# Optimization experiments

Measured on AMD Instinct MI355X. Metric: run time of the kernel, lower is better.

Reference implementation:

```python
import jax, jax.numpy as jnp
import numpy as np

EMB = 1024
HEADS = 16
QKV = 64
INNER = 2816  # 256 * ceil(2*1024*4/3 / 256)


def rms_norm(x, w, eps=1e-6):
    xf = x.astype(jnp.float32)
    n = xf * jax.lax.rsqrt(jnp.mean(xf * xf, axis=-1, keepdims=True) + eps)
    return n.astype(x.dtype) * w


def setup_inputs() -> dict:
    key = jax.random.key(0)
    ks = jax.random.split(key, 12)
    s = 0.02
    return {
        "x": jax.random.normal(ks[0], (4, 2048, EMB), dtype=jnp.float32),
        "Wq": jax.random.normal(ks[1], (HEADS * QKV, EMB), dtype=jnp.float32) * s,
        "Wk": jax.random.normal(ks[2], (HEADS * QKV, EMB), dtype=jnp.float32) * s,
        "Wv": jax.random.normal(ks[3], (HEADS * QKV, EMB), dtype=jnp.float32) * s,
        "Wc": jax.random.normal(ks[4], (EMB, HEADS * QKV), dtype=jnp.float32) * s,
        "bc": jnp.zeros((EMB,), dtype=jnp.float32),
        "g1": jnp.ones((EMB,), dtype=jnp.float32),
        "g2": jnp.ones((EMB,), dtype=jnp.float32),
        "L1": jax.random.normal(ks[5], (INNER, EMB), dtype=jnp.float32) * s,
        "L2": jax.random.normal(ks[6], (INNER, EMB), dtype=jnp.float32) * s,
        "L3": jax.random.normal(ks[7], (EMB, INNER), dtype=jnp.float32) * s,
    }


def reference(x, Wq, Wk, Wv, Wc, bc, g1, g2, L1, L2, L3):
    B, N, D = x.shape
    # QKV projections (torch Linear: y = x @ W.T), split into heads: [B,H,N,dk]
    q = (x @ Wq.T).reshape(B, N, HEADS, QKV).transpose(0, 2, 1, 3)
    k = (x @ Wk.T).reshape(B, N, HEADS, QKV).transpose(0, 2, 1, 3)
    v = (x @ Wv.T).reshape(B, N, HEADS, QKV).transpose(0, 2, 1, 3)
    # attention: explicit score matrix [B,H,N,N]
    score = jnp.einsum("bhnd,bhmd->bhnm", q, k) / jnp.sqrt(jnp.float32(QKV))
    weights = jax.nn.softmax(score, axis=-1)
    out = jnp.einsum("bhnm,bhmd->bhnd", weights, v)
    out = out.transpose(0, 2, 1, 3).reshape(B, N, HEADS * QKV)
    mha = out @ Wc.T + bc
    h = rms_norm(x + mha, g1)
    # parallel gated MLP: silu(h@L1.T) * (h@L2.T) @ L3.T
    ff = (jax.nn.silu(h @ L1.T) * (h @ L2.T)) @ L3.T
    return rms_norm(h + ff, g2)
```

## Files before the change

kernel.cpp:

```cpp
#include <hip/hip_runtime.h>
#include <hip/hip_bf16.h>


#define EMB   1024
#define HEADS 16
#define DK    64
#define INNER 2816
#define BATCH 4
#define NTOK  2048
#define MROWS (BATCH * NTOK)

#define QSCALE 0.18033688011112042f

typedef short bf16x8 __attribute__((ext_vector_type(8)));
typedef short s16x4  __attribute__((ext_vector_type(4)));
typedef float f32x4  __attribute__((ext_vector_type(4)));

typedef const void __attribute__((address_space(1)))* gas_cvp;
typedef void       __attribute__((address_space(3)))* las_vp;

__device__ __forceinline__ short to_bf16(float f) {
  union { float f; unsigned u; } x; x.f = f;
  unsigned r = x.u + 0x7FFFu + ((x.u >> 16) & 1u);
  return (short)(r >> 16);
}

__device__ __forceinline__ unsigned cvt_pk_bf16(float a, float b) {
  unsigned r;
  asm("v_cvt_pk_bf16_f32 %0, %1, %2" : "=v"(r) : "v"(a), "v"(b));
  return r;
}

__device__ __forceinline__ void gld16(void* lds, const void* g) {
  __builtin_amdgcn_global_load_lds((gas_cvp)g, (las_vp)lds, 16, 0, 0);
}

__global__ __launch_bounds__(256, 4)
void cvtk(const float* __restrict__ s, short* __restrict__ d, int n4) {
  int i = blockIdx.x * 256 + threadIdx.x;
  if (i < n4) {
    float4 v = ((const float4*)s)[i];
    s16x4 o;
    o[0] = to_bf16(v.x); o[1] = to_bf16(v.y);
    o[2] = to_bf16(v.z); o[3] = to_bf16(v.w);
    ((s16x4*)d)[i] = o;
  }
}

__global__ __launch_bounds__(256, 4)
void cvt_inter(const float* __restrict__ L1, const float* __restrict__ L2,
               short* __restrict__ d) {
  int i = blockIdx.x * 256 + threadIdx.x;
  if (i >= INNER * 256) return;
  int row = i >> 8, c4 = i & 255;
  float4 v1 = ((const float4*)L1)[i];
  float4 v2 = ((const float4*)L2)[i];
  s16x4 o1, o2;
  o1[0]=to_bf16(v1.x); o1[1]=to_bf16(v1.y); o1[2]=to_bf16(v1.z); o1[3]=to_bf16(v1.w);
  o2[0]=to_bf16(v2.x); o2[1]=to_bf16(v2.y); o2[2]=to_bf16(v2.z); o2[3]=to_bf16(v2.w);
  ((s16x4*)d)[(size_t)(2 * row) * 256 + c4]     = o1;
  ((s16x4*)d)[(size_t)(2 * row + 1) * 256 + c4] = o2;
}

template<int MODE>
__global__ __launch_bounds__(256, 2)
void gemm_bt(const short* __restrict__ A, const short* __restrict__ Bw,
             int M, int N, int K,
             void* __restrict__ out0, void* __restrict__ out1,
             void* __restrict__ out2,
             const float* __restrict__ aux0, const float* __restrict__ aux1)
{
  __shared__ short At[128 * 64];
  __shared__ short Bt[128 * 64];
  const int t = threadIdx.x;
  const int lane = t & 63;
  const int l15 = lane & 15, lhi = lane >> 4;
  const int w  = t >> 6;
  const int wm = (w >> 1) << 6;
  const int wn = (w & 1) << 6;
  const int tilesN = N >> 7;
  const int m0 = (blockIdx.x / tilesN) << 7;
  const int n0 = (blockIdx.x % tilesN) << 7;

  const int r = t >> 3;
  const int p = t & 7;
  const int psrc = p ^ (r & 7);
  const short* Ag = A  + (size_t)(m0 + r) * K + psrc * 8;
  const short* Bg = Bw + (size_t)(n0 + r) * K + psrc * 8;

  f32x4 acc[4][4];
  const f32x4 fz = {0.f, 0.f, 0.f, 0.f};
#pragma unroll
  for (int i = 0; i < 4; i++)
#pragma unroll
    for (int j = 0; j < 4; j++) acc[i][j] = fz;

  int aoff[2][4], boff[2][4];
#pragma unroll
  for (int kk = 0; kk < 2; kk++)
#pragma unroll
    for (int mt = 0; mt < 4; mt++) {
      int ra = wm + mt * 16 + l15;
      aoff[kk][mt] = ra * 128 + ((kk * 64 + lhi * 16) ^ ((ra & 7) << 4));
      int rb = wn + mt * 16 + l15;
      boff[kk][mt] = rb * 128 + ((kk * 64 + lhi * 16) ^ ((rb & 7) << 4));
    }

  for (int k0 = 0; k0 < K; k0 += 64) {
#pragma unroll
    for (int i = 0; i < 4; i++) {
      gld16((char*)At + t * 16 + i * 4096, Ag + (size_t)i * 32 * K + k0);
      gld16((char*)Bt + t * 16 + i * 4096, Bg + (size_t)i * 32 * K + k0);
    }
    __syncthreads();
#pragma unroll
    for (int kk = 0; kk < 2; kk++) {
      bf16x8 a[4], b[4];
#pragma unroll
      for (int mt = 0; mt < 4; mt++)
        a[mt] = *(const bf16x8*)((const char*)At + aoff[kk][mt]);
#pragma unroll
      for (int nt = 0; nt < 4; nt++)
        b[nt] = *(const bf16x8*)((const char*)Bt + boff[kk][nt]);
#pragma unroll
      for (int mt = 0; mt < 4; mt++)
#pragma unroll
        for (int nt = 0; nt < 4; nt++)
          acc[mt][nt] = __builtin_amdgcn_mfma_f32_16x16x32_bf16(
              a[mt], b[nt], acc[mt][nt], 0, 0, 0);
    }
    __syncthreads();
  }

#pragma unroll
  for (int mt = 0; mt < 4; mt++) {
#pragma unroll
    for (int nt = 0; nt < 4; nt++) {
      const int mb = m0 + wm + mt * 16 + lhi * 4;
      const int n  = n0 + wn + nt * 16 + l15;
      if constexpr (MODE == 0) {
        const int which = n >> 10, c = n & 1023;
        if (which == 2) {
          const int hh = c >> 6, dd = c & 63;
          const int bb = mb >> 11, tok = mb & 2047;
          s16x4 pk;
#pragma unroll
          for (int j = 0; j < 4; j++) pk[j] = to_bf16(acc[mt][nt][j]);
          *(s16x4*)((short*)out2 +
                    (size_t)((bb * HEADS + hh) * DK + dd) * NTOK + tok) = pk;
        } else {
          short* dst = (which == 0) ? (short*)out0 : (short*)out1;
          const float scl = (which == 0) ? QSCALE : 1.0f;
#pragma unroll
          for (int j = 0; j < 4; j++)
            dst[(size_t)(mb + j) * 1024 + c] = to_bf16(acc[mt][nt][j] * scl);
        }
      } else if constexpr (MODE == 1) {
#pragma unroll
        for (int j = 0; j < 4; j++) {
          size_t idx = (size_t)(mb + j) * 1024 + n;
          ((float*)out0)[idx] = acc[mt][nt][j] + aux1[n] + aux0[idx];
        }
      } else if constexpr (MODE == 2) {
#pragma unroll
        for (int j = 0; j < 4; j++) {
          float v0 = acc[mt][nt][j];
          float v1 = __shfl_xor(v0, 1);
          if ((lane & 1) == 0) {
            float su = v0 / (1.f + __expf(-v0));
            ((short*)out0)[(size_t)(mb + j) * INNER + (n >> 1)] =
                to_bf16(su * v1);
          }
        }
      } else {
#pragma unroll
        for (int j = 0; j < 4; j++) {
          size_t idx = (size_t)(mb + j) * 1024 + n;
          ((float*)out0)[idx] = acc[mt][nt][j] + aux0[idx];
        }
      }
    }
  }
}

__global__ __launch_bounds__(256, 3)
void attn_k(const short* __restrict__ qb, const short* __restrict__ kb,
            const short* __restrict__ vtb, short* __restrict__ ob)
{
  __shared__ short Kt[2][64 * 64];
  __shared__ short Vt[2][64 * 64];
  __shared__ short Pt[128 * 68];
  const int t = threadIdx.x;
  const int lane = t & 63;
  const int l15 = lane & 15, lhi = lane >> 4;
  const int w = t >> 6;
  const int bh = blockIdx.x;
  const int b = bh >> 4, h = bh & 15;
  const int q0 = blockIdx.y << 7;

  bf16x8 aq[2][2];
#pragma unroll
  for (int s = 0; s < 2; s++) {
    const short* qp = qb + (size_t)(b * NTOK + q0 + w * 32 + s * 16 + l15) * EMB
                         + h * DK + lhi * 8;
    aq[s][0] = *(const bf16x8*)qp;
    aq[s][1] = *(const bf16x8*)(qp + 32);
  }

  f32x4 acc[2][4];
  const f32x4 fz = {0.f, 0.f, 0.f, 0.f};
#pragma unroll
  for (int s = 0; s < 2; s++)
#pragma unroll
    for (int dt = 0; dt < 4; dt++) acc[s][dt] = fz;
  float m_run[2] = {-1e30f, -1e30f};
  float l_run[2] = {0.f, 0.f};

  const int r = t >> 3, p = t & 7;
  const int psrc = p ^ (r & 7);
  const short* kg = kb  + (size_t)(b * NTOK + r) * EMB + h * DK + psrc * 8;
  const short* vg = vtb + (size_t)(bh * DK + r) * NTOK + psrc * 8;

  int kvoff[4][2];
#pragma unroll
  for (int x = 0; x < 4; x++)
#pragma unroll
    for (int kk = 0; kk < 2; kk++) {
      int row = x * 16 + l15;
      kvoff[x][kk] = row * 128 + ((kk * 64 + lhi * 16) ^ ((row & 7) << 4));
    }
  int pw[2][4], pr[2][2];
#pragma unroll
  for (int s = 0; s < 2; s++) {
    const int prow = w * 32 + s * 16 + l15;
#pragma unroll
    for (int kvt = 0; kvt < 4; kvt++) pw[s][kvt] = prow * 136 + kvt * 32 + lhi * 8;
#pragma unroll
    for (int kk = 0; kk < 2; kk++)   pr[s][kk]  = prow * 136 + kk * 64 + lhi * 16;
  }

  auto stage = [&](short* Kd, short* Vd, int kv0) {
    const short* ks = kg + (size_t)kv0 * EMB;
    const short* vs = vg + kv0;
    gld16(Kd + t * 8,        ks);
    gld16(Kd + t * 8 + 2048, ks + (size_t)32 * EMB);
    gld16(Vd + t * 8,        vs);
    gld16(Vd + t * 8 + 2048, vs + (size_t)32 * NTOK);
  };

  auto do_set = [&](f32x4 (&sv)[4], float& mr, float& lr, f32x4 (&ac)[4],
                    const int (&pwo)[4]) {
    float pm = sv[0][0];
#pragma unroll
    for (int kvt = 0; kvt < 4; kvt++)
#pragma unroll
      for (int j = 0; j < 4; j++) pm = fmaxf(pm, sv[kvt][j]);
    if (__any(pm > mr + 8.0f)) {
      pm = fmaxf(pm, __shfl_xor(pm, 16));
      pm = fmaxf(pm, __shfl_xor(pm, 32));
      const float mnew = fmaxf(mr, pm);
      const float al = exp2f(mr - mnew);
      lr *= al;
#pragma unroll
      for (int dt = 0; dt < 4; dt++)
#pragma unroll
        for (int j = 0; j < 4; j++) ac[dt][j] *= al;
      mr = mnew;
    }
    float ls = 0.f;
#pragma unroll
    for (int kvt = 0; kvt < 4; kvt++)
#pragma unroll
      for (int j = 0; j < 4; j++) {
        float pe = exp2f(sv[kvt][j] - mr);
        sv[kvt][j] = pe;
        ls += pe;
      }
    lr += ls;
#pragma unroll
    for (int kvt = 0; kvt < 4; kvt++) {
      uint2 u;
      u.x = cvt_pk_bf16(sv[kvt][0], sv[kvt][1]);
      u.y = cvt_pk_bf16(sv[kvt][2], sv[kvt][3]);
      *(uint2*)((char*)Pt + pwo[kvt]) = u;
    }
  };

  auto compute = [&](const short* Kb_, const short* Vb_) {
    const char* Kb = (const char*)Kb_;
    const char* Vb = (const char*)Vb_;
    bf16x8 kf[4][2];
#pragma unroll
    for (int x = 0; x < 4; x++)
#pragma unroll
      for (int kk = 0; kk < 2; kk++)
        kf[x][kk] = *(const bf16x8*)(Kb + kvoff[x][kk]);
    f32x4 s0[4], s1[4];
    __builtin_amdgcn_s_setprio(1);
#pragma unroll
    for (int kvt = 0; kvt < 4; kvt++) {
      s0[kvt] = __builtin_amdgcn_mfma_f32_16x16x32_bf16(kf[kvt][0], aq[0][0], fz, 0, 0, 0);
      s0[kvt] = __builtin_amdgcn_mfma_f32_16x16x32_bf16(kf[kvt][1], aq[0][1], s0[kvt], 0, 0, 0);
      s1[kvt] = __builtin_amdgcn_mfma_f32_16x16x32_bf16(kf[kvt][0], aq[1][0], fz, 0, 0, 0);
      s1[kvt] = __builtin_amdgcn_mfma_f32_16x16x32_bf16(kf[kvt][1], aq[1][1], s1[kvt], 0, 0, 0);
    }
    __builtin_amdgcn_s_setprio(0);
    do_set(s0, m_run[0], l_run[0], acc[0], pw[0]);
    do_set(s1, m_run[1], l_run[1], acc[1], pw[1]);
    bf16x8 vf[4][2];
#pragma unroll
    for (int dt = 0; dt < 4; dt++)
#pragma unroll
      for (int kk = 0; kk < 2; kk++)
        vf[dt][kk] = *(const bf16x8*)(Vb + kvoff[dt][kk]);
    bf16x8 pb0[2], pb1[2];
#pragma unroll
    for (int kk = 0; kk < 2; kk++) {
      pb0[kk] = *(const bf16x8*)((const char*)Pt + pr[0][kk]);
      pb1[kk] = *(const bf16x8*)((const char*)Pt + pr[1][kk]);
    }
    __builtin_amdgcn_s_setprio(1);
#pragma unroll
    for (int dt = 0; dt < 4; dt++) {
#pragma unroll
      for (int kk = 0; kk < 2; kk++)
        acc[0][dt] = __builtin_amdgcn_mfma_f32_16x16x32_bf16(vf[dt][kk], pb0[kk], acc[0][dt], 0, 0, 0);
#pragma unroll
      for (int kk = 0; kk < 2; kk++)
        acc[1][dt] = __builtin_amdgcn_mfma_f32_16x16x32_bf16(vf[dt][kk], pb1[kk], acc[1][dt], 0, 0, 0);
    }
    __builtin_amdgcn_s_setprio(0);
  };

  stage(Kt[0], Vt[0], 0);
  for (int it = 0; it < 32; it += 2) {
    stage(Kt[1], Vt[1], (it + 1) * 64);
    asm volatile("s_waitcnt vmcnt(4)" ::: "memory");
    __builtin_amdgcn_s_barrier();
    compute(Kt[0], Vt[0]);
    __builtin_amdgcn_s_barrier();
    if (it + 2 < 32) {
      stage(Kt[0], Vt[0], (it + 2) * 64);
      asm volatile("s_waitcnt vmcnt(4)" ::: "memory");
    } else {
      asm volatile("s_waitcnt vmcnt(0)" ::: "memory");
    }
    __builtin_amdgcn_s_barrier();
    compute(Kt[1], Vt[1]);
    __builtin_amdgcn_s_barrier();
  }

#pragma unroll
  for (int s = 0; s < 2; s++) {
    float lt = l_run[s];
    lt += __shfl_xor(lt, 16);
    lt += __shfl_xor(lt, 32);
    const float inv = 1.f / lt;
    short* op = ob + (size_t)(b * NTOK + q0 + w * 32 + s * 16 + l15) * EMB + h * DK;
#pragma unroll
    for (int dt = 0; dt < 4; dt++) {
      s16x4 pk;
#pragma unroll
      for (int j = 0; j < 4; j++) pk[j] = to_bf16(acc[s][dt][j] * inv);
      *(s16x4*)(op + dt * 16 + lhi * 4) = pk;
    }
  }
}

template<bool WB>
__global__ __launch_bounds__(256, 4)
void rmsnorm_k(const float* __restrict__ in, const float* __restrict__ gw,
               float* __restrict__ of, short* __restrict__ ob)
{
  const int row = blockIdx.x;
  const int t = threadIdx.x;
  const float4 v = ((const float4*)(in + (size_t)row * EMB))[t];
  float ss = v.x * v.x + v.y * v.y + v.z * v.z + v.w * v.w;
#pragma unroll
  for (int off = 1; off < 64; off <<= 1) ss += __shfl_xor(ss, off);
  __shared__ float red[4];
  if ((t & 63) == 0) red[t >> 6] = ss;
  __syncthreads();
  float tot = red[0] + red[1] + red[2] + red[3];
  const float rinv = rsqrtf(tot * (1.f / EMB) + 1e-6f);
  const float4 g4 = ((const float4*)gw)[t];
  float4 o;
  o.x = v.x * rinv * g4.x; o.y = v.y * rinv * g4.y;
  o.z = v.z * rinv * g4.z; o.w = v.w * rinv * g4.w;
  ((float4*)(of + (size_t)row * EMB))[t] = o;
  if (WB) {
    s16x4 pk;
    pk[0] = to_bf16(o.x); pk[1] = to_bf16(o.y);
    pk[2] = to_bf16(o.z); pk[3] = to_bf16(o.w);
    ((s16x4*)(ob + (size_t)row * EMB))[t] = pk;
  }
}

extern "C" void kernel_launch(void* const* d_in, const int* in_sizes, int n_in,
                              void* d_out, int out_size, void* d_ws, size_t ws_size,
                              hipStream_t stream)
{
  const float* x  = (const float*)d_in[0];
  const float* Wq = (const float*)d_in[1];
  const float* Wk = (const float*)d_in[2];
  const float* Wv = (const float*)d_in[3];
  const float* Wc = (const float*)d_in[4];
  const float* bc = (const float*)d_in[5];
  const float* g1 = (const float*)d_in[6];
  const float* g2 = (const float*)d_in[7];
  const float* L1 = (const float*)d_in[8];
  const float* L2 = (const float*)d_in[9];
  const float* L3 = (const float*)d_in[10];
  float* out = (float*)d_out;

  char* ws = (char*)d_ws;
  size_t o = 0;
  auto take = [&](size_t bytes) -> char* {
    char* pp = ws + o;
    o += (bytes + 255) & ~(size_t)255;
    return pp;
  };
  short* xb   = (short*)take((size_t)MROWS * EMB * 2);
  short* wqkv = (short*)take((size_t)3072 * 1024 * 2);
  short* wcb  = (short*)take((size_t)1024 * 1024 * 2);
  short* l12  = (short*)take((size_t)5632 * 1024 * 2);
  short* l3b  = (short*)take((size_t)1024 * 2816 * 2);
  short* q    = (short*)take((size_t)MROWS * EMB * 2);
  short* k    = (short*)take((size_t)MROWS * EMB * 2);
  short* v    = (short*)take((size_t)MROWS * EMB * 2);
  short* attn = (short*)take((size_t)MROWS * EMB * 2);
  float* t1   = (float*)take((size_t)MROWS * EMB * 4);
  float* h32  = (float*)take((size_t)MROWS * EMB * 4);
  short* hb   = (short*)take((size_t)MROWS * EMB * 2);
  short* gated = q;
  float* t2    = t1;

  cvtk<<<MROWS * EMB / 4 / 256, 256, 0, stream>>>(x, xb, MROWS * EMB / 4);
  cvtk<<<1024 * 1024 / 4 / 256, 256, 0, stream>>>(Wq, wqkv, 1024 * 1024 / 4);
  cvtk<<<1024 * 1024 / 4 / 256, 256, 0, stream>>>(Wk, wqkv + 1024 * 1024, 1024 * 1024 / 4);
  cvtk<<<1024 * 1024 / 4 / 256, 256, 0, stream>>>(Wv, wqkv + 2 * 1024 * 1024, 1024 * 1024 / 4);
  cvtk<<<1024 * 1024 / 4 / 256, 256, 0, stream>>>(Wc, wcb, 1024 * 1024 / 4);
  cvt_inter<<<INNER, 256, 0, stream>>>(L1, L2, l12);
  cvtk<<<1024 * 2816 / 4 / 256, 256, 0, stream>>>(L3, l3b, 1024 * 2816 / 4);

  gemm_bt<0><<<64 * 24, 256, 0, stream>>>(xb, wqkv, MROWS, 3072, 1024,
                                          q, k, v, nullptr, nullptr);
  attn_k<<<dim3(64, 16), 256, 0, stream>>>(q, k, v, attn);
  gemm_bt<1><<<64 * 8, 256, 0, stream>>>(attn, wcb, MROWS, 1024, 1024,
                                         t1, nullptr, nullptr, x, bc);
  rmsnorm_k<true><<<MROWS, 256, 0, stream>>>(t1, g1, h32, hb);
  gemm_bt<2><<<64 * 44, 256, 0, stream>>>(hb, l12, MROWS, 5632, 1024,
                                          gated, nullptr, nullptr, nullptr, nullptr);
  gemm_bt<3><<<64 * 8, 256, 0, stream>>>(gated, l3b, MROWS, 1024, 2816,
                                         t2, nullptr, nullptr, h32, nullptr);
  rmsnorm_k<false><<<MROWS, 256, 0, stream>>>(t2, g2, out, nullptr);
}
```

Baseline: 442.3 us.

## Add 256x256-tile 8-wave pipelined GEMM for QKV and gated-MLP projections

Introduces gemm256, a 512-thread kernel with 256x256 output tiles and double-buffered LDS. It interleaves quarter-tile global loads with MFMA quadrants and raises wave priority around MFMA bursts. It also remaps blocks into eight grouped chunks for cache locality. The QKV and L1/L2 GEMMs move to it to improve data reuse and overlap loads with compute, while the smaller N=1024 GEMMs stay on the old 128x128 kernel. In exchange it uses much more LDS and registers per block, and the hand-placed waitcnt and barrier schedule is fragile.

Result: slower. 462.3 us (+4.5%).

```diff
diff --git a/kernel.cpp b/kernel.cpp
--- a/kernel.cpp
+++ b/kernel.cpp
@@ -66,8 +66,7 @@
 __global__ __launch_bounds__(256, 2)
 void gemm_bt(const short* __restrict__ A, const short* __restrict__ Bw,
              int M, int N, int K,
-             void* __restrict__ out0, void* __restrict__ out1,
-             void* __restrict__ out2,
+             void* __restrict__ out0,
              const float* __restrict__ aux0, const float* __restrict__ aux1)
 {
   __shared__ short At[128 * 64];
@@ -138,6 +137,168 @@
     for (int nt = 0; nt < 4; nt++) {
       const int mb = m0 + wm + mt * 16 + lhi * 4;
       const int n  = n0 + wn + nt * 16 + l15;
+      if constexpr (MODE == 1) {
+#pragma unroll
+        for (int j = 0; j < 4; j++) {
+          size_t idx = (size_t)(mb + j) * 1024 + n;
+          ((float*)out0)[idx] = acc[mt][nt][j] + aux1[n] + aux0[idx];
+        }
+      } else {
+#pragma unroll
+        for (int j = 0; j < 4; j++) {
+          size_t idx = (size_t)(mb + j) * 1024 + n;
+          ((float*)out0)[idx] = acc[mt][nt][j] + aux0[idx];
+        }
+      }
+    }
+  }
+}
+
+#define G256_LDA(buf, mh) do {                                              \
+  const char* _b = (const char*)&lds[buf][0][0] + (mh) * 8192;              \
+  _Pragma("unroll") for (int mt = 0; mt < 4; mt++)                          \
+    _Pragma("unroll") for (int kk = 0; kk < 2; kk++)                        \
+      af[mt][kk] = *(const bf16x8*)(_b + aoff[mt][kk]);                     \
+} while (0)
+
+#define G256_LDB(buf, nh) do {                                              \
+  const char* _b = (const char*)&lds[buf][1][0] + (nh) * 4096;              \
+  _Pragma("unroll") for (int nt = 0; nt < 2; nt++)                          \
+    _Pragma("unroll") for (int kk = 0; kk < 2; kk++)                        \
+      bN[nh][nt][kk] = *(const bf16x8*)(_b + boff[nt][kk]);                 \
+} while (0)
+
+#define G256_MFQ(mh, nh) do {                                               \
+  __builtin_amdgcn_s_setprio(1);                                            \
+  _Pragma("unroll") for (int mt = 0; mt < 4; mt++)                          \
+    _Pragma("unroll") for (int nt = 0; nt < 2; nt++)                        \
+      _Pragma("unroll") for (int kk = 0; kk < 2; kk++)                      \
+        acc[(mh)*4+mt][(nh)*2+nt] = __builtin_amdgcn_mfma_f32_16x16x32_bf16(\
+            af[mt][kk], bN[nh][nt][kk], acc[(mh)*4+mt][(nh)*2+nt], 0, 0, 0);\
+  __builtin_amdgcn_s_setprio(0);                                            \
+} while (0)
+
+#define G256_SYNC() do {                                                    \
+  __builtin_amdgcn_s_barrier();                                             \
+  asm volatile("s_waitcnt lgkmcnt(0)" ::: "memory");                        \
+  __builtin_amdgcn_sched_barrier(0);                                        \
+} while (0)
+
+template<int MODE>
+__global__ __launch_bounds__(512, 2)
+void gemm256(const short* __restrict__ A, const short* __restrict__ Bw,
+             int M, int N, int K,
+             void* __restrict__ out0, void* __restrict__ out1,
+             void* __restrict__ out2)
+{
+  __shared__ short lds[2][2][16384];
+  const int t = threadIdx.x;
+  const int lane = t & 63;
+  const int l15 = lane & 15, lhi = lane >> 4;
+  const int w = t >> 6;
+  const int wr = w >> 2, wc = w & 3;
+
+  const int chunk = gridDim.x >> 3;
+  const int bid = blockIdx.x;
+  const int wg = (bid & 7) * chunk + (bid >> 3);
+  const int tilesM = M >> 8;
+  const int m0 = (wg % tilesM) << 8;
+  const int n0 = (wg / tilesM) << 8;
+
+  const int r = t >> 3, p = t & 7;
+  const int psrc = p ^ (r & 7);
+  const short* Ag = A  + (size_t)(m0 + r) * K + psrc * 8;
+  const short* Bg = Bw + (size_t)(n0 + r) * K + psrc * 8;
+  const int NT = K >> 6;
+
+  f32x4 acc[8][4];
+  const f32x4 fz = {0.f, 0.f, 0.f, 0.f};
+#pragma unroll
+  for (int i = 0; i < 8; i++)
+#pragma unroll
+    for (int j = 0; j < 4; j++) acc[i][j] = fz;
+
+  int aoff[4][2], boff[2][2];
+#pragma unroll
+  for (int mt = 0; mt < 4; mt++)
+#pragma unroll
+    for (int kk = 0; kk < 2; kk++)
+      aoff[mt][kk] = (wr * 128 + mt * 16 + l15) * 128 +
+                     ((kk * 64 + lhi * 16) ^ ((l15 & 7) << 4));
+#pragma unroll
+  for (int nt = 0; nt < 2; nt++)
+#pragma unroll
+    for (int kk = 0; kk < 2; kk++)
+      boff[nt][kk] = (wc * 64 + nt * 16 + l15) * 128 +
+                     ((kk * 64 + lhi * 16) ^ ((l15 & 7) << 4));
+
+  bf16x8 af[4][2], bN[2][2][2];
+
+  auto stg = [&](int buf, int kt, int hh) {
+    const int sel = hh >> 1, hf = hh & 1;
+    short* dst = &lds[buf][sel][hf * 8192] + t * 8;
+    const short* src = (sel ? Bg : Ag) + (size_t)(hf * 128) * K + kt * 64;
+    gld16(dst, src);
+    gld16(dst + 4096, src + (size_t)64 * K);
+  };
+
+  stg(0, 0, 0); stg(0, 0, 1); stg(0, 0, 2); stg(0, 0, 3);
+  stg(1, 1, 0);
+  asm volatile("s_waitcnt vmcnt(2)" ::: "memory");
+  __builtin_amdgcn_s_barrier();
+
+  for (int i = 0; i < NT / 2; ++i) {
+    const int T1 = 2 * i + 1, T2 = 2 * i + 2, T3 = 2 * i + 3;
+    G256_LDA(0, 0); G256_LDB(0, 0);
+    stg(1, T1, 1);
+    G256_SYNC();
+    G256_MFQ(0, 0);
+    __builtin_amdgcn_s_barrier();
+    G256_LDB(0, 1);
+    stg(1, T1, 2);
+    G256_SYNC();
+    G256_MFQ(0, 1);
+    __builtin_amdgcn_s_barrier();
+    G256_LDA(0, 1);
+    stg(1, T1, 3);
+    G256_SYNC();
+    G256_MFQ(1, 1);
+    __builtin_amdgcn_s_barrier();
+    if (T2 < NT) stg(0, T2, 0);
+    G256_SYNC();
+    G256_MFQ(1, 0);
+    if (T2 < NT) asm volatile("s_waitcnt vmcnt(2)" ::: "memory");
+    else         asm volatile("s_waitcnt vmcnt(0)" ::: "memory");
+    __builtin_amdgcn_s_barrier();
+    G256_LDA(1, 0); G256_LDB(1, 0);
+    if (T2 < NT) stg(0, T2, 1);
+    G256_SYNC();
+    G256_MFQ(0, 0);
+    __builtin_amdgcn_s_barrier();
+    G256_LDB(1, 1);
+    if (T2 < NT) stg(0, T2, 2);
+    G256_SYNC();
+    G256_MFQ(0, 1);
+    __builtin_amdgcn_s_barrier();
+    G256_LDA(1, 1);
+    if (T2 < NT) stg(0, T2, 3);
+    G256_SYNC();
+    G256_MFQ(1, 1);
+    __builtin_amdgcn_s_barrier();
+    if (T3 < NT) stg(1, T3, 0);
+    G256_SYNC();
+    G256_MFQ(1, 0);
+    if (T3 < NT) asm volatile("s_waitcnt vmcnt(2)" ::: "memory");
+    else         asm volatile("s_waitcnt vmcnt(0)" ::: "memory");
+    __builtin_amdgcn_s_barrier();
+  }
+
+#pragma unroll
+  for (int mt = 0; mt < 8; mt++) {
+#pragma unroll
+    for (int nt = 0; nt < 4; nt++) {
+      const int mb = m0 + wr * 128 + mt * 16 + lhi * 4;
+      const int n  = n0 + wc * 64 + nt * 16 + l15;
       if constexpr (MODE == 0) {
         const int which = n >> 10, c = n & 1023;
         if (which == 2) {
@@ -155,13 +316,7 @@
           for (int j = 0; j < 4; j++)
             dst[(size_t)(mb + j) * 1024 + c] = to_bf16(acc[mt][nt][j] * scl);
         }
-      } else if constexpr (MODE == 1) {
-#pragma unroll
-        for (int j = 0; j < 4; j++) {
-          size_t idx = (size_t)(mb + j) * 1024 + n;
-          ((float*)out0)[idx] = acc[mt][nt][j] + aux1[n] + aux0[idx];
-        }
-      } else if constexpr (MODE == 2) {
+      } else {
 #pragma unroll
         for (int j = 0; j < 4; j++) {
           float v0 = acc[mt][nt][j];
@@ -171,12 +326,6 @@
             ((short*)out0)[(size_t)(mb + j) * INNER + (n >> 1)] =
                 to_bf16(su * v1);
           }
-        }
-      } else {
-#pragma unroll
-        for (int j = 0; j < 4; j++) {
-          size_t idx = (size_t)(mb + j) * 1024 + n;
-          ((float*)out0)[idx] = acc[mt][nt][j] + aux0[idx];
         }
       }
     }
@@ -443,15 +592,15 @@
   cvt_inter<<<INNER, 256, 0, stream>>>(L1, L2, l12);
   cvtk<<<1024 * 2816 / 4 / 256, 256, 0, stream>>>(L3, l3b, 1024 * 2816 / 4);
 
-  gemm_bt<0><<<64 * 24, 256, 0, stream>>>(xb, wqkv, MROWS, 3072, 1024,
-                                          q, k, v, nullptr, nullptr);
+  gemm256<0><<<32 * 12, 512, 0, stream>>>(xb, wqkv, MROWS, 3072, 1024,
+                                          q, k, v);
   attn_k<<<dim3(64, 16), 256, 0, stream>>>(q, k, v, attn);
   gemm_bt<1><<<64 * 8, 256, 0, stream>>>(attn, wcb, MROWS, 1024, 1024,
-                                         t1, nullptr, nullptr, x, bc);
+                                         t1, x, bc);
   rmsnorm_k<true><<<MROWS, 256, 0, stream>>>(t1, g1, h32, hb);
-  gemm_bt<2><<<64 * 44, 256, 0, stream>>>(hb, l12, MROWS, 5632, 1024,
-                                          gated, nullptr, nullptr, nullptr, nullptr);
+  gemm256<2><<<32 * 22, 512, 0, stream>>>(hb, l12, MROWS, 5632, 1024,
+                                          gated, nullptr, nullptr);
   gemm_bt<3><<<64 * 8, 256, 0, stream>>>(gated, l3b, MROWS, 1024, 2816,
-                                         t2, nullptr, nullptr, h32, nullptr);
+                                         t2, h32, nullptr);
   rmsnorm_k<false><<<MROWS, 256, 0, stream>>>(t2, g2, out, nullptr);
 }
```
